# Kernel optimization log

Hardware: AMD Instinct MI355X
Metric: run time of the kernel (lower is better)

## Reference

```python
import jax, jax.numpy as jnp
import numpy as np

N = 13627        # n_nodes (from negative_sampling call in source)
E_EDGES = 504378 # n_edges
F_IN = 64
H1, H2, LIN_H = 300, 100, 100  # CONFIG HIDDEN_1/HIDDEN_2/LINEAR_HIDDEN


def setup_inputs() -> dict:
    key = jax.random.key(0)
    ks = jax.random.split(key, 10)
    x = jax.random.normal(ks[0], (N, F_IN), jnp.float32)
    edge_index = jax.random.randint(ks[1], (2, E_EDGES), 0, N, dtype=jnp.int64)
    neg_edge_index = jax.random.randint(ks[2], (2, E_EDGES), 0, N, dtype=jnp.int64)
    def w(k, shape):
        return jax.random.normal(k, shape, jnp.float32) * 0.05
    return dict(
        x=x, edge_index=edge_index, neg_edge_index=neg_edge_index,
        W1=w(ks[3], (2, F_IN, H1)), b1=jnp.zeros((H1,), jnp.float32),
        W2=w(ks[4], (2, H1, H2)), b2=jnp.zeros((H2,), jnp.float32),
        W3=w(ks[5], (2, H2, 1)), b3=jnp.zeros((1,), jnp.float32),
        linW1=w(ks[6], (F_IN, LIN_H)), linb1=jnp.zeros((LIN_H,), jnp.float32),
        linW2=w(ks[7], (F_IN, LIN_H)), linb2=jnp.zeros((LIN_H,), jnp.float32),
        c1=jnp.array([0.5], jnp.float32), c2=jnp.array([0.5], jnp.float32),
    )


def _cheb_norm(edge_index, n):
    # PyG ChebConv sym normalization with lambda_max=2: Lhat = L - I,
    # off-diagonal entries -deg[src]^-1/2 * deg[dst]^-1/2, diagonal 0.
    src, dst = edge_index[0], edge_index[1]
    deg = jax.ops.segment_sum(jnp.ones(src.shape, jnp.float32), src, num_segments=n)
    dinv = jnp.where(deg > 0, jax.lax.rsqrt(jnp.maximum(deg, 1.0)), 0.0)
    return -dinv[src] * dinv[dst]


def _cheb_conv(x, W, b, src, dst, norm, n):
    # K=2: out = Tx0 @ W[0] + Tx1 @ W[1] + b, with Tx1 = Lhat @ x (gather-scale-scatter)
    tx1 = jax.ops.segment_sum(norm[:, None] * x[src], dst, num_segments=n)
    return x @ W[0] + tx1 @ W[1] + b


def reference(x, edge_index, neg_edge_index, W1, b1, W2, b2, W3, b3,
              linW1, linb1, linW2, linb2, c1, c2):
    n = x.shape[0]
    src, dst = edge_index[0], edge_index[1]
    norm = _cheb_norm(edge_index, n)
    h = jax.nn.relu(_cheb_conv(x, W1, b1, src, dst, norm, n))
    x1 = jax.nn.relu(_cheb_conv(h, W2, b2, src, dst, norm, n))
    xo = x1 + jax.nn.relu(x @ linW1 + linb1)
    z = x1 + jax.nn.relu(x @ linW2 + linb2)
    pos = jax.nn.sigmoid(jnp.sum(z[edge_index[0]] * z[edge_index[1]], axis=1))
    pos_loss = -jnp.mean(jnp.log(pos + 1e-15))
    neg = jax.nn.sigmoid(jnp.sum(z[neg_edge_index[0]] * z[neg_edge_index[1]], axis=1))
    neg_loss = -jnp.mean(jnp.log(1.0 - neg + 1e-15))
    r_loss = pos_loss + neg_loss
    out = _cheb_conv(xo, W3, b3, src, dst, norm, n)
    return out, r_loss, c1, c2
```

## Files before the change

### kernel.cpp

```cpp
#include <hip/hip_runtime.h>
#include <math.h>


typedef unsigned short ushort_t;
typedef float v2f __attribute__((ext_vector_type(2)));
typedef short bf16x8 __attribute__((ext_vector_type(8)));
typedef float f32x4 __attribute__((ext_vector_type(4)));

#define GBM 64
#define GBN 64
#define GBK 32
#define LDK 72
#define HB  256
#define PACKN 6816

__device__ inline short f2bf(float f) {
    unsigned u = __float_as_uint(f);
    u += 0x7fff + ((u >> 16) & 1);
    return (short)(u >> 16);
}
__device__ inline float bflo(unsigned w) { return __uint_as_float(w << 16); }
__device__ inline float bfhi(unsigned w) { return __uint_as_float(w & 0xffff0000u); }

__device__ inline float dot16fp8(uint4 ra, uint4 rb) {
    float dot = 0.0f;
    v2f fa, fb;
    fa = __builtin_amdgcn_cvt_pk_f32_fp8(ra.x, false);
    fb = __builtin_amdgcn_cvt_pk_f32_fp8(rb.x, false);
    dot += fa.x * fb.x + fa.y * fb.y;
    fa = __builtin_amdgcn_cvt_pk_f32_fp8(ra.x, true);
    fb = __builtin_amdgcn_cvt_pk_f32_fp8(rb.x, true);
    dot += fa.x * fb.x + fa.y * fb.y;
    fa = __builtin_amdgcn_cvt_pk_f32_fp8(ra.y, false);
    fb = __builtin_amdgcn_cvt_pk_f32_fp8(rb.y, false);
    dot += fa.x * fb.x + fa.y * fb.y;
    fa = __builtin_amdgcn_cvt_pk_f32_fp8(ra.y, true);
    fb = __builtin_amdgcn_cvt_pk_f32_fp8(rb.y, true);
    dot += fa.x * fb.x + fa.y * fb.y;
    fa = __builtin_amdgcn_cvt_pk_f32_fp8(ra.z, false);
    fb = __builtin_amdgcn_cvt_pk_f32_fp8(rb.z, false);
    dot += fa.x * fb.x + fa.y * fb.y;
    fa = __builtin_amdgcn_cvt_pk_f32_fp8(ra.z, true);
    fb = __builtin_amdgcn_cvt_pk_f32_fp8(rb.z, true);
    dot += fa.x * fb.x + fa.y * fb.y;
    fa = __builtin_amdgcn_cvt_pk_f32_fp8(ra.w, false);
    fb = __builtin_amdgcn_cvt_pk_f32_fp8(rb.w, false);
    dot += fa.x * fb.x + fa.y * fb.y;
    fa = __builtin_amdgcn_cvt_pk_f32_fp8(ra.w, true);
    fb = __builtin_amdgcn_cvt_pk_f32_fp8(rb.w, true);
    dot += fa.x * fb.x + fa.y * fb.y;
    return dot;
}

__device__ inline float loss_term(float d, int y) {
    float sg = __builtin_amdgcn_rcpf(1.0f + __expf(-d));
    return y ? __logf(1.0f - sg + 1e-15f) : __logf(sg + 1e-15f);
}

__global__ __launch_bounds__(512) void hist_both_x_kernel(
    const int* __restrict__ ei, const float* __restrict__ x,
    int* __restrict__ degp, int* __restrict__ cntp,
    ushort_t* __restrict__ xb, int Nn, int E) {
    __shared__ int lhs[PACKN];
    __shared__ int lhd[PACKN];
    for (int i = threadIdx.x; i < PACKN; i += 512) { lhs[i] = 0; lhd[i] = 0; }
    __syncthreads();
    const int b = blockIdx.x;
    const int chunk = (E + HB - 1) / HB;
    const int e0 = b * chunk;
    const int e1 = (e0 + chunk < E) ? (e0 + chunk) : E;
    for (int e = e0 + threadIdx.x; e < e1; e += 512) {
        int s = ei[e], d = ei[E + e];
        atomicAdd(&lhs[s >> 1], 1 << ((s & 1) << 4));
        atomicAdd(&lhd[d >> 1], 1 << ((d & 1) << 4));
    }
    __syncthreads();
    int* ds = degp + (size_t)b * PACKN;
    int* cs = cntp + (size_t)b * PACKN;
    for (int i = threadIdx.x; i < PACKN; i += 512) { ds[i] = lhs[i]; cs[i] = lhd[i]; }
    const int rpb = (Nn + HB - 1) / HB;
    const int r0 = b * rpb;
    const int r1 = (r0 + rpb < Nn) ? (r0 + rpb) : Nn;
    for (int i = r0 * 64 + (int)threadIdx.x; i < r1 * 64; i += 512)
        xb[i] = (ushort_t)f2bf(x[i]);
}

__global__ void merge_kernel(const int* __restrict__ degp, const int* __restrict__ cntp,
                             ushort_t* __restrict__ off, int Nal,
                             float* __restrict__ dinv, int* __restrict__ rowptr,
                             float* __restrict__ acc, int n) {
    int tid = blockIdx.x * blockDim.x + threadIdx.x;
    if (tid == 0) {
        rowptr[0] = 0;
        acc[0] = 0.0f; acc[1] = 0.0f; acc[2] = 0.0f; acc[3] = 0.0f;
    }
    int v = tid >> 2, qq = tid & 3;
    if (v >= n) return;
    const int vh = v >> 1, sh = (v & 1) << 4;
    const int b0 = qq * (HB / 4), b1 = b0 + HB / 4;
    int dsum = 0, csum = 0;
    for (int b = b0; b < b1; ++b) {
        dsum += (degp[(size_t)b * PACKN + vh] >> sh) & 0xffff;
        csum += (cntp[(size_t)b * PACKN + vh] >> sh) & 0xffff;
    }
    int dtot = dsum;
    dtot += __shfl_xor(dtot, 1, 64);
    dtot += __shfl_xor(dtot, 2, 64);
    int inc = csum;
    int t = __shfl_up(inc, 1, 64); if (qq >= 1) inc += t;
    t = __shfl_up(inc, 2, 64);     if (qq >= 2) inc += t;
    int ex = inc - csum;
    if (qq == 0) dinv[v] = (dtot > 0) ? (1.0f / sqrtf((float)dtot)) : 0.0f;
    if (qq == 3) rowptr[v + 1] = inc;
    int run = ex;
    for (int b = b0; b < b1; ++b) {
        off[(size_t)b * Nal + v] = (ushort_t)run;
        run += (cntp[(size_t)b * PACKN + vh] >> sh) & 0xffff;
    }
}

__global__ void scan_kernel(int* __restrict__ rowptr, int n) {
    __shared__ int wsum[16];
    __shared__ int carry_s;
    if (threadIdx.x == 0) carry_s = 0;
    __syncthreads();
    int nchunk = (n + 1023) / 1024;
    int wid = threadIdx.x >> 6, lane = threadIdx.x & 63;
    for (int c = 0; c < nchunk; ++c) {
        int i = c * 1024 + threadIdx.x;
        int v = (i < n) ? rowptr[i + 1] : 0;
        int s = v;
        for (int off = 1; off < 64; off <<= 1) {
            int t = __shfl_up(s, off, 64);
            if (lane >= off) s += t;
        }
        if (lane == 63) wsum[wid] = s;
        __syncthreads();
        if (wid == 0 && lane < 16) {
            int wsv = wsum[lane];
            for (int off = 1; off < 16; off <<= 1) {
                int t = __shfl_up(wsv, off, 64);
                if (lane >= off) wsv += t;
            }
            wsum[lane] = wsv;
        }
        __syncthreads();
        int base = carry_s + (wid > 0 ? wsum[wid - 1] : 0);
        int inc = base + s;
        if (i < n) rowptr[i + 1] = inc;
        __syncthreads();
        if (threadIdx.x == 1023) carry_s = inc;
        __syncthreads();
    }
}

__global__ __launch_bounds__(512) void fill_lds_kernel(
    const int* __restrict__ ei, const float* __restrict__ dinv,
    const int* __restrict__ rowptr, const ushort_t* __restrict__ off, int Nal,
    int* __restrict__ colidx, float* __restrict__ wnorm, int E) {
    __shared__ int lh[PACKN];
    for (int i = threadIdx.x; i < PACKN; i += 512) lh[i] = 0;
    __syncthreads();
    const int b = blockIdx.x;
    const int chunk = (E + HB - 1) / HB;
    const int e0 = b * chunk;
    const int e1 = (e0 + chunk < E) ? (e0 + chunk) : E;
    const ushort_t* boff = off + (size_t)b * Nal;
    for (int e = e0 + threadIdx.x; e < e1; e += 512) {
        int s = ei[e], d = ei[E + e];
        int sh = (d & 1) << 4;
        int old = atomicAdd(&lh[d >> 1], 1 << sh);
        int rank = (old >> sh) & 0xffff;
        int slot = rowptr[d] + (int)boff[d] + rank;
        colidx[slot] = s;
        wnorm[slot] = -dinv[s] * dinv[d];
    }
}

__global__ void xt_kernel(const ushort_t* __restrict__ xb, const int* __restrict__ rowptr,
                          const int* __restrict__ colidx, const float* __restrict__ wnorm,
                          ushort_t* __restrict__ XTb, int n) {
    int node = (blockIdx.x * blockDim.x + threadIdx.x) >> 6;
    if (node >= n) return;
    int lane = threadIdx.x & 63;
    int grp = lane >> 4;
    int l = lane & 15;
    int j0 = rowptr[node], j1 = rowptr[node + 1];
    float a0 = 0, a1 = 0, a2 = 0, a3 = 0;
    int j = j0 + grp;
    if (j < j1) {
        float w = wnorm[j];
        int c = colidx[j];
        uint2 r = ((const uint2*)(xb + (size_t)c * 64))[l];
        for (;;) {
            int jn = j + 4;
            bool more = jn < j1;
            float wn = 0.0f;
            uint2 rn = r;
            if (more) {
                int cn = colidx[jn];
                wn = wnorm[jn];
                rn = ((const uint2*)(xb + (size_t)cn * 64))[l];
            }
            a0 += w * bflo(r.x); a1 += w * bfhi(r.x);
            a2 += w * bflo(r.y); a3 += w * bfhi(r.y);
            if (!more) break;
            j = jn; w = wn; r = rn;
        }
    }
    a0 += __shfl_xor(a0, 16, 64); a0 += __shfl_xor(a0, 32, 64);
    a1 += __shfl_xor(a1, 16, 64); a1 += __shfl_xor(a1, 32, 64);
    a2 += __shfl_xor(a2, 16, 64); a2 += __shfl_xor(a2, 32, 64);
    a3 += __shfl_xor(a3, 16, 64); a3 += __shfl_xor(a3, 32, 64);
    if (grp == 0) {
        uint2 xv = ((const uint2*)(xb + (size_t)node * 64))[l];
        *(uint2*)&XTb[(size_t)node * 128 + l * 4] = xv;
        uint2 p;
        p.x = (unsigned)(unsigned short)f2bf(a0) | ((unsigned)(unsigned short)f2bf(a1) << 16);
        p.y = (unsigned)(unsigned short)f2bf(a2) | ((unsigned)(unsigned short)f2bf(a3) << 16);
        *(uint2*)&XTb[(size_t)node * 128 + 64 + l * 4] = p;
    }
}

__global__ __launch_bounds__(256) void gemm_mfma(
    const ushort_t* __restrict__ Abf, int lda,
    const float* __restrict__ B0, const float* __restrict__ B1, const float* __restrict__ B2,
    const float* __restrict__ bias0, const float* __restrict__ bias1, const float* __restrict__ bias2,
    int split, int split2, int klim1,
    float* __restrict__ C, int ldc, ushort_t* __restrict__ Cbf, int ldcbf,
    int cbf_mode, int Nrows, int K, int Ncols, int relu) {
    __shared__ short As[GBM * LDK];
    __shared__ short Bs[GBN * LDK];
    const int bm = blockIdx.y * GBM, bn = blockIdx.x * GBN;
    const int tid = threadIdx.x;
    const int w = tid >> 6, l = tid & 63;
    const int wm = (w >> 1) * 32, wn = (w & 1) * 32;
    const int lr = l & 15;
    const int kg = l >> 4;
    const int arow = tid >> 2, aseg = tid & 3;
    const int bcol = tid & 63, bk2 = (tid >> 6) * 2;

    const int arowg = bm + arow;
    const int bcolg = bn + bcol;
    const float* Bsrc = nullptr;
    int ldb = 1, Klim = K;
    if (bcolg < split)                            { Bsrc = B0 + bcolg; ldb = split; Klim = K; }
    else if (bcolg < split2 && bcolg < Ncols)     { Bsrc = B1 + (bcolg - split); ldb = split2 - split; Klim = klim1; }
    else if (bcolg < Ncols)                       { Bsrc = B2 + (bcolg - split2); ldb = Ncols - split2; Klim = klim1; }

    f32x4 acc00 = {0,0,0,0}, acc01 = {0,0,0,0}, acc10 = {0,0,0,0}, acc11 = {0,0,0,0};

    for (int k0 = 0; k0 < K; k0 += GBK) {
        {
            int kk = k0 + aseg * 8;
            bf16x8 v;
            if (arowg < Nrows && kk + 7 < K) {
                v = *(const bf16x8*)&Abf[(size_t)arowg * lda + kk];
            } else {
#pragma unroll
                for (int i = 0; i < 8; ++i)
                    v[i] = (arowg < Nrows && kk + i < K)
                         ? (short)Abf[(size_t)arowg * lda + kk + i] : (short)0;
            }
            *(bf16x8*)&As[arow * LDK + aseg * 8] = v;
        }
#pragma unroll
        for (int q = 0; q < 4; ++q) {
            int k = q * 8 + bk2;
            unsigned pw = 0u;
            if (Bsrc) {
                float f0 = (k0 + k < Klim) ? Bsrc[(size_t)(k0 + k) * ldb] : 0.0f;
                float f1 = (k0 + k + 1 < Klim) ? Bsrc[(size_t)(k0 + k + 1) * ldb] : 0.0f;
                pw = (unsigned)(unsigned short)f2bf(f0)
                   | ((unsigned)(unsigned short)f2bf(f1) << 16);
            }
            *(unsigned*)&Bs[bcol * LDK + k] = pw;
        }
        __syncthreads();
        bf16x8 a0 = *(const bf16x8*)&As[(wm + lr) * LDK + kg * 8];
        bf16x8 a1 = *(const bf16x8*)&As[(wm + 16 + lr) * LDK + kg * 8];
        bf16x8 b0 = *(const bf16x8*)&Bs[(wn + lr) * LDK + kg * 8];
        bf16x8 b1 = *(const bf16x8*)&Bs[(wn + 16 + lr) * LDK + kg * 8];
        acc00 = __builtin_amdgcn_mfma_f32_16x16x32_bf16(a0, b0, acc00, 0, 0, 0);
        acc01 = __builtin_amdgcn_mfma_f32_16x16x32_bf16(a0, b1, acc01, 0, 0, 0);
        acc10 = __builtin_amdgcn_mfma_f32_16x16x32_bf16(a1, b0, acc10, 0, 0, 0);
        acc11 = __builtin_amdgcn_mfma_f32_16x16x32_bf16(a1, b1, acc11, 0, 0, 0);
        __syncthreads();
    }
#pragma unroll
    for (int i = 0; i < 2; ++i) {
        int rbase = bm + wm + i * 16 + kg * 4;
#pragma unroll
        for (int j = 0; j < 2; ++j) {
            int col = bn + wn + j * 16 + lr;
            if (col >= Ncols) continue;
            float bv;
            if (col < split)       bv = bias0 ? bias0[col] : 0.0f;
            else if (col < split2) bv = bias1 ? bias1[col - split] : 0.0f;
            else                   bv = bias2 ? bias2[col - split2] : 0.0f;
            f32x4 a = (i == 0) ? (j == 0 ? acc00 : acc01) : (j == 0 ? acc10 : acc11);
#pragma unroll
            for (int r = 0; r < 4; ++r) {
                int row = rbase + r;
                if (row >= Nrows) continue;
                float o = a[r] + bv;
                if (cbf_mode == 3) {
                    if (col < split)
                        Cbf[(size_t)row * ldcbf + col] = (ushort_t)f2bf(fmaxf(o, 0.0f));
                    else
                        C[(size_t)row * ldc + (col - split)] = o;
                } else if (cbf_mode == 2) {
                    if (relu) o = fmaxf(o, 0.0f);
                    Cbf[(size_t)row * ldcbf + col] = (ushort_t)f2bf(o);
                } else if (cbf_mode == 1 && col >= split) {
                    Cbf[(size_t)row * 128 + (col - split)] = (ushort_t)f2bf(o);
                } else {
                    if (relu) o = fmaxf(o, 0.0f);
                    C[(size_t)row * ldc + col] = o;
                }
            }
        }
    }
}

__global__ void segsum_combine1_kernel(const ushort_t* __restrict__ hb,
                                       const int* __restrict__ rowptr, const int* __restrict__ colidx,
                                       const float* __restrict__ wnorm,
                                       const float* __restrict__ G2a, const float* __restrict__ b2,
                                       float* __restrict__ x1, int n) {
    int node = (blockIdx.x * blockDim.x + threadIdx.x) >> 6;
    if (node >= n) return;
    int lane = threadIdx.x & 63;
    int grp = lane >> 4;
    int l = lane & 15;
    int j0 = rowptr[node], j1 = rowptr[node + 1];
    float acc[8] = {};
    int j = j0 + grp;
    if (j < j1) {
        float w = wnorm[j];
        int c = colidx[j];
        uint4 r = ((const uint4*)(hb + (size_t)c * 128))[l];
        for (;;) {
            int jn = j + 4;
            bool more = jn < j1;
            float wn = 0.0f;
            uint4 rn = r;
            if (more) {
                int cn = colidx[jn];
                wn = wnorm[jn];
                rn = ((const uint4*)(hb + (size_t)cn * 128))[l];
            }
            acc[0] += w * bflo(r.x); acc[1] += w * bfhi(r.x);
            acc[2] += w * bflo(r.y); acc[3] += w * bfhi(r.y);
            acc[4] += w * bflo(r.z); acc[5] += w * bfhi(r.z);
            acc[6] += w * bflo(r.w); acc[7] += w * bfhi(r.w);
            if (!more) break;
            j = jn; w = wn; r = rn;
        }
    }
#pragma unroll
    for (int k = 0; k < 8; ++k) {
        acc[k] += __shfl_xor(acc[k], 16, 64);
        acc[k] += __shfl_xor(acc[k], 32, 64);
    }
    if (grp == 0) {
        int f = l * 8;
        if (f < 100) {
            float4 g0 = *(const float4*)&G2a[(size_t)node * 100 + f];
            float4 bv0 = *(const float4*)&b2[f];
            float4 o0;
            o0.x = fmaxf(g0.x + acc[0] + bv0.x, 0.0f);
            o0.y = fmaxf(g0.y + acc[1] + bv0.y, 0.0f);
            o0.z = fmaxf(g0.z + acc[2] + bv0.z, 0.0f);
            o0.w = fmaxf(g0.w + acc[3] + bv0.w, 0.0f);
            *(float4*)&x1[(size_t)node * 100 + f] = o0;
            if (f + 8 <= 100) {
                float4 g1 = *(const float4*)&G2a[(size_t)node * 100 + f + 4];
                float4 bv1 = *(const float4*)&b2[f + 4];
                float4 o1;
                o1.x = fmaxf(g1.x + acc[4] + bv1.x, 0.0f);
                o1.y = fmaxf(g1.y + acc[5] + bv1.y, 0.0f);
                o1.z = fmaxf(g1.z + acc[6] + bv1.z, 0.0f);
                o1.w = fmaxf(g1.w + acc[7] + bv1.w, 0.0f);
                *(float4*)&x1[(size_t)node * 100 + f + 4] = o1;
            }
        }
    }
}

__global__ void combine2_kernel(const float* __restrict__ S, const float* __restrict__ x1,
                                const float* __restrict__ w3b,
                                float* __restrict__ xo, unsigned* __restrict__ zf,
                                float* __restrict__ sv, int n) {
    int idx = blockIdx.x * blockDim.x + threadIdx.x;
    if (idx >= n * 32) return;
    int i = idx >> 5, q = idx & 31;
    unsigned w = 0u;
    float part = 0.0f;
    if (q < 25) {
        float4 s1 = *(const float4*)&S[(size_t)i * 200 + q * 4];
        float4 s2 = *(const float4*)&S[(size_t)i * 200 + 100 + q * 4];
        float4 xv = *(const float4*)&x1[(size_t)i * 100 + q * 4];
        float4 a, b;
        a.x = xv.x + fmaxf(s1.x, 0.0f); a.y = xv.y + fmaxf(s1.y, 0.0f);
        a.z = xv.z + fmaxf(s1.z, 0.0f); a.w = xv.w + fmaxf(s1.w, 0.0f);
        b.x = xv.x + fmaxf(s2.x, 0.0f); b.y = xv.y + fmaxf(s2.y, 0.0f);
        b.z = xv.z + fmaxf(s2.z, 0.0f); b.w = xv.w + fmaxf(s2.w, 0.0f);
        *(float4*)&xo[(size_t)i * 100 + q * 4] = a;
        w = (unsigned)__builtin_amdgcn_cvt_pk_fp8_f32(b.x, b.y, 0, false);
        w = (unsigned)__builtin_amdgcn_cvt_pk_fp8_f32(b.z, b.w, (int)w, true);
        float4 wv = *(const float4*)&w3b[q * 4];
        part = a.x * wv.x + a.y * wv.y + a.z * wv.z + a.w * wv.w;
    }
    zf[(size_t)i * 32 + q] = w;
#pragma unroll
    for (int off = 16; off > 0; off >>= 1)
        part += __shfl_xor(part, off, 32);
    if (q == 0) sv[i] = part;
}

__global__ __launch_bounds__(256) void edge_loss_fp8_kernel(
    const unsigned* __restrict__ zf, const int* __restrict__ ei,
    const int* __restrict__ nei, int E, float* __restrict__ accv) {
    const int y = blockIdx.y;
    const int* __restrict__ lst = y ? nei : ei;
    const int l = threadIdx.x & 7;
    const int g = (blockIdx.x * blockDim.x + threadIdx.x) >> 3;
    const int ng = (gridDim.x * blockDim.x) >> 3;
    const int stride2 = 2 * ng;
    float s = 0.0f;
    const int gA = g, gB = g + ng;
    int niterA = (gA < E) ? ((E - 1 - gA) / stride2 + 1) : 0;
    int niterB = (gB < E) ? ((E - 1 - gB) / stride2 + 1) : 0;
    if (niterA > 0) {
        int eB0 = (gB < E) ? gB : (E - 1);
        int eA1 = (gA + stride2 < E) ? (gA + stride2) : (E - 1);
        int eB1 = (gB + stride2 < E) ? (gB + stride2) : (E - 1);
        int aA0 = lst[gA], bA0 = lst[E + gA];
        int aB0 = lst[eB0], bB0 = lst[E + eB0];
        int aA1 = lst[eA1], bA1 = lst[E + eA1];
        int aB1 = lst[eB1], bB1 = lst[E + eB1];
        uint4 raA = *(const uint4*)&zf[(size_t)aA0 * 32 + l * 4];
        uint4 rbA = *(const uint4*)&zf[(size_t)bA0 * 32 + l * 4];
        uint4 raB = *(const uint4*)&zf[(size_t)aB0 * 32 + l * 4];
        uint4 rbB = *(const uint4*)&zf[(size_t)bB0 * 32 + l * 4];
        for (int t = 0; t < niterA; ++t) {
            int eA2 = gA + (t + 2) * stride2; eA2 = (eA2 < E) ? eA2 : (E - 1);
            int eB2 = gB + (t + 2) * stride2; eB2 = (eB2 < E) ? eB2 : (E - 1);
            int aA2 = lst[eA2], bA2 = lst[E + eA2];
            int aB2 = lst[eB2], bB2 = lst[E + eB2];
            uint4 raA1 = *(const uint4*)&zf[(size_t)aA1 * 32 + l * 4];
            uint4 rbA1 = *(const uint4*)&zf[(size_t)bA1 * 32 + l * 4];
            uint4 raB1 = *(const uint4*)&zf[(size_t)aB1 * 32 + l * 4];
            uint4 rbB1 = *(const uint4*)&zf[(size_t)bB1 * 32 + l * 4];
            float dA = dot16fp8(raA, rbA);
            float dB = dot16fp8(raB, rbB);
            dA += __shfl_xor(dA, 1, 8); dB += __shfl_xor(dB, 1, 8);
            dA += __shfl_xor(dA, 2, 8); dB += __shfl_xor(dB, 2, 8);
            dA += __shfl_xor(dA, 4, 8); dB += __shfl_xor(dB, 4, 8);
            if (l == 0) {
                s += loss_term(dA, y);
                if (t < niterB) s += loss_term(dB, y);
            }
            aA1 = aA2; bA1 = bA2; aB1 = aB2; bB1 = bB2;
            raA = raA1; rbA = rbA1; raB = raB1; rbB = rbB1;
        }
    }
    __shared__ float red[256];
    red[threadIdx.x] = s;
    __syncthreads();
    for (int st = 128; st > 0; st >>= 1) {
        if (threadIdx.x < st) red[threadIdx.x] += red[threadIdx.x + st];
        __syncthreads();
    }
    if (threadIdx.x == 0) atomicAdd(&accv[y], red[0]);
}

__global__ void out_finalize_kernel(const float* __restrict__ xo, const float* __restrict__ W3,
                                    const float* __restrict__ b3, const int* __restrict__ rowptr,
                                    const int* __restrict__ colidx, const float* __restrict__ wnorm,
                                    const float* __restrict__ sv, const float* __restrict__ accv,
                                    const float* __restrict__ c1, const float* __restrict__ c2,
                                    float* __restrict__ out, int n, int E) {
    int i = blockIdx.x * blockDim.x + threadIdx.x;
    if (i == 0) {
        out[n]     = -(accv[0] + accv[1]) / (float)E;
        out[n + 1] = c1[0];
        out[n + 2] = c2[0];
    }
    if (i >= n) return;
    const float4* a = (const float4*)(xo + (size_t)i * 100);
    const float4* wv = (const float4*)W3;
    float acc = b3[0];
#pragma unroll
    for (int q = 0; q < 25; ++q) {
        float4 va = a[q], vw = wv[q];
        acc += va.x * vw.x + va.y * vw.y + va.z * vw.z + va.w * vw.w;
    }
    int j1 = rowptr[i + 1];
    for (int j = rowptr[i]; j < j1; ++j)
        acc += wnorm[j] * sv[colidx[j]];
    out[i] = acc;
}

extern "C" void kernel_launch(void* const* d_in, const int* in_sizes, int n_in,
                              void* d_out, int out_size, void* d_ws, size_t ws_size,
                              hipStream_t stream) {
    (void)n_in; (void)out_size; (void)ws_size;
    const float* x   = (const float*)d_in[0];
    const int*   ei  = (const int*)d_in[1];
    const int*   nei = (const int*)d_in[2];
    const float* W1  = (const float*)d_in[3];
    const float* b1  = (const float*)d_in[4];
    const float* W2  = (const float*)d_in[5];
    const float* b2  = (const float*)d_in[6];
    const float* W3  = (const float*)d_in[7];
    const float* b3  = (const float*)d_in[8];
    const float* lw1 = (const float*)d_in[9];
    const float* lb1 = (const float*)d_in[10];
    const float* lw2 = (const float*)d_in[11];
    const float* lb2 = (const float*)d_in[12];
    const float* c1  = (const float*)d_in[13];
    const float* c2  = (const float*)d_in[14];

    const int Nn = in_sizes[0] / 64;
    const int E  = in_sizes[1] / 2;

    const size_t Nal = ((size_t)Nn + 5) & ~(size_t)3;
    const size_t Eal = ((size_t)E + 3) & ~(size_t)3;
    const int LDH = 304;

    float* ws       = (float*)d_ws;
    float* acc      = ws;
    float* dinv     = acc + 4;
    int*   rowptr   = (int*)(dinv + Nal);
    int*   colidx   = rowptr + Nal;
    float* wnorm    = (float*)(colidx + Eal);
    int*   degp     = (int*)(wnorm + Eal);
    int*   cntp     = degp + (size_t)HB * PACKN;
    ushort_t* offus = (ushort_t*)(cntp + (size_t)HB * PACKN);
    ushort_t* xb    = offus + (size_t)HB * Nal;
    ushort_t* XTb   = xb + (size_t)Nn * 64;
    ushort_t* hb    = XTb + (size_t)Nn * 128;
    float* G2a      = (float*)(hb + (size_t)Nn * LDH);
    float* x1       = G2a + (size_t)Nn * 100;
    float* xo       = x1 + (size_t)Nn * 100;
    float* S        = xo + (size_t)Nn * 100;
    size_t zoff     = (size_t)(S + (size_t)Nn * 200 - ws);
    zoff = (zoff + 31) & ~(size_t)31;
    unsigned* zf    = (unsigned*)(ws + zoff);
    size_t hoff2    = zoff + (size_t)Nn * 32 + 63;
    hoff2 &= ~(size_t)63;
    ushort_t* hWb   = (ushort_t*)(ws + hoff2);
    float* sv       = ws + hoff2 + (size_t)Nn * 64;
    const int MB = (Nn + GBM - 1) / GBM;

    hist_both_x_kernel<<<HB, 512, 0, stream>>>(ei, x, degp, cntp, xb, Nn, E);
    merge_kernel<<<(4 * Nn + 255) / 256, 256, 0, stream>>>(degp, cntp, offus, (int)Nal,
                                                           dinv, rowptr, acc, Nn);
    scan_kernel<<<1, 1024, 0, stream>>>(rowptr, Nn);
    fill_lds_kernel<<<HB, 512, 0, stream>>>(ei, dinv, rowptr, offus, (int)Nal,
                                            colidx, wnorm, E);

    xt_kernel<<<(Nn + 3) / 4, 256, 0, stream>>>(xb, rowptr, colidx, wnorm, XTb, Nn);
    gemm_mfma<<<dim3(8, MB), 256, 0, stream>>>(
        XTb, 128, W1, lw1, lw2, b1, lb1, lb2,
        300, 400, 64, S, 200, hb, LDH, 3, Nn, 128, 500, 1);

    gemm_mfma<<<dim3(4, MB), 256, 0, stream>>>(
        hb, LDH, W2, W2 + 300 * 100, W2 + 300 * 100, nullptr, nullptr, nullptr,
        100, 200, 300, G2a, 100, hWb, 0, 1, Nn, 300, 200, 0);
    segsum_combine1_kernel<<<(Nn + 3) / 4, 256, 0, stream>>>(hWb, rowptr, colidx, wnorm,
                                                             G2a, b2, x1, Nn);

    combine2_kernel<<<(Nn * 32 + 255) / 256, 256, 0, stream>>>(S, x1, W3 + 100,
                                                               xo, zf, sv, Nn);

    edge_loss_fp8_kernel<<<dim3(1024, 2), 256, 0, stream>>>(zf, ei, nei, E, acc);

    out_finalize_kernel<<<(Nn + 255) / 256, 256, 0, stream>>>(
        xo, W3, b3, rowptr, colidx, wnorm, sv, acc, c1, c2, (float*)d_out, Nn, E);
}
```

Baseline: 206.8 us.

## Pre-pack weights to transposed bf16 and drop LDS staging in GEMMs

Adds a kernel that converts W1, the two linear weights and W2 once into padded, transposed bf16 matrices, with a fused bias vector. The GEMM is rewritten so each wave loads its MFMA operands straight from global memory, with no shared-memory staging and no barriers. This removes the strided fp32 weight loads and the per-tile bf16 conversion that every block used to repeat. In exchange it adds an extra launch, pads the hidden buffer to 320 columns, and relies on caches to absorb the operand loads that waves now fetch redundantly.

```diff
diff --git a/kernel.cpp b/kernel.cpp
--- a/kernel.cpp
+++ b/kernel.cpp
@@ -7,12 +7,9 @@
 typedef short bf16x8 __attribute__((ext_vector_type(8)));
 typedef float f32x4 __attribute__((ext_vector_type(4)));
 
-#define GBM 64
-#define GBN 64
-#define GBK 32
-#define LDK 72
 #define HB  256
 #define PACKN 6816
+#define LDH 320
 
 __device__ inline short f2bf(float f) {
     unsigned u = __float_as_uint(f);
@@ -55,6 +52,38 @@
 __device__ inline float loss_term(float d, int y) {
     float sg = __builtin_amdgcn_rcpf(1.0f + __expf(-d));
     return y ? __logf(1.0f - sg + 1e-15f) : __logf(sg + 1e-15f);
+}
+
+__global__ void pack_weights_kernel(const float* __restrict__ W1, const float* __restrict__ b1,
+                                    const float* __restrict__ lw1, const float* __restrict__ lb1,
+                                    const float* __restrict__ lw2, const float* __restrict__ lb2,
+                                    const float* __restrict__ W2,
+                                    ushort_t* __restrict__ BtA, float* __restrict__ ba,
+                                    ushort_t* __restrict__ BtB) {
+    int tid = blockIdx.x * blockDim.x + threadIdx.x;
+    int stride = gridDim.x * blockDim.x;
+    for (int i = tid; i < 576 * 128; i += stride) {
+        int r = i >> 7, k = i & 127;
+        float v = 0.0f;
+        if (r < 300) v = W1[(size_t)k * 300 + r];
+        else if (r >= 320 && r < 420) { if (k < 64) v = lw1[k * 100 + (r - 320)]; }
+        else if (r >= 420 && r < 520) { if (k < 64) v = lw2[k * 100 + (r - 420)]; }
+        BtA[i] = (ushort_t)f2bf(v);
+    }
+    for (int i = tid; i < 576; i += stride) {
+        float v = 0.0f;
+        if (i < 300) v = b1[i];
+        else if (i >= 320 && i < 420) v = lb1[i - 320];
+        else if (i >= 420 && i < 520) v = lb2[i - 420];
+        ba[i] = v;
+    }
+    for (int i = tid; i < 256 * 320; i += stride) {
+        int r = i / 320, k = i - r * 320;
+        float v = 0.0f;
+        if (k < 300 && r < 200)
+            v = (r < 100) ? W2[(size_t)k * 100 + r] : W2[30000 + (size_t)k * 100 + (r - 100)];
+        BtB[i] = (ushort_t)f2bf(v);
+    }
 }
 
 __global__ __launch_bounds__(512) void hist_both_x_kernel(
@@ -222,70 +251,32 @@
     }
 }
 
-__global__ __launch_bounds__(256) void gemm_mfma(
+__global__ __launch_bounds__(256) void gemm_direct(
     const ushort_t* __restrict__ Abf, int lda,
-    const float* __restrict__ B0, const float* __restrict__ B1, const float* __restrict__ B2,
-    const float* __restrict__ bias0, const float* __restrict__ bias1, const float* __restrict__ bias2,
-    int split, int split2, int klim1,
+    const ushort_t* __restrict__ Bt, int ldbt,
+    const float* __restrict__ bias,
     float* __restrict__ C, int ldc, ushort_t* __restrict__ Cbf, int ldcbf,
-    int cbf_mode, int Nrows, int K, int Ncols, int relu) {
-    __shared__ short As[GBM * LDK];
-    __shared__ short Bs[GBN * LDK];
-    const int bm = blockIdx.y * GBM, bn = blockIdx.x * GBN;
+    int mode, int split, int Nrows, int Kp, int Ncols) {
+    const int bm = blockIdx.y * 64, bn = blockIdx.x * 64;
     const int tid = threadIdx.x;
     const int w = tid >> 6, l = tid & 63;
     const int wm = (w >> 1) * 32, wn = (w & 1) * 32;
-    const int lr = l & 15;
-    const int kg = l >> 4;
-    const int arow = tid >> 2, aseg = tid & 3;
-    const int bcol = tid & 63, bk2 = (tid >> 6) * 2;
-
-    const int arowg = bm + arow;
-    const int bcolg = bn + bcol;
-    const float* Bsrc = nullptr;
-    int ldb = 1, Klim = K;
-    if (bcolg < split)                            { Bsrc = B0 + bcolg; ldb = split; Klim = K; }
-    else if (bcolg < split2 && bcolg < Ncols)     { Bsrc = B1 + (bcolg - split); ldb = split2 - split; Klim = klim1; }
-    else if (bcolg < Ncols)                       { Bsrc = B2 + (bcolg - split2); ldb = Ncols - split2; Klim = klim1; }
-
+    const int lr = l & 15, kg = l >> 4;
+    const ushort_t* pa0 = Abf + (size_t)(bm + wm + lr) * lda + kg * 8;
+    const ushort_t* pa1 = pa0 + (size_t)16 * lda;
+    const ushort_t* pb0 = Bt + (size_t)(bn + wn + lr) * ldbt + kg * 8;
+    const ushort_t* pb1 = pb0 + (size_t)16 * ldbt;
     f32x4 acc00 = {0,0,0,0}, acc01 = {0,0,0,0}, acc10 = {0,0,0,0}, acc11 = {0,0,0,0};
-
-    for (int k0 = 0; k0 < K; k0 += GBK) {
-        {
-            int kk = k0 + aseg * 8;
-            bf16x8 v;
-            if (arowg < Nrows && kk + 7 < K) {
-                v = *(const bf16x8*)&Abf[(size_t)arowg * lda + kk];
-            } else {
-#pragma unroll
-                for (int i = 0; i < 8; ++i)
-                    v[i] = (arowg < Nrows && kk + i < K)
-                         ? (short)Abf[(size_t)arowg * lda + kk + i] : (short)0;
-            }
-            *(bf16x8*)&As[arow * LDK + aseg * 8] = v;
-        }
-#pragma unroll
-        for (int q = 0; q < 4; ++q) {
-            int k = q * 8 + bk2;
-            unsigned pw = 0u;
-            if (Bsrc) {
-                float f0 = (k0 + k < Klim) ? Bsrc[(size_t)(k0 + k) * ldb] : 0.0f;
-                float f1 = (k0 + k + 1 < Klim) ? Bsrc[(size_t)(k0 + k + 1) * ldb] : 0.0f;
-                pw = (unsigned)(unsigned short)f2bf(f0)
-                   | ((unsigned)(unsigned short)f2bf(f1) << 16);
-            }
-            *(unsigned*)&Bs[bcol * LDK + k] = pw;
-        }
-        __syncthreads();
-        bf16x8 a0 = *(const bf16x8*)&As[(wm + lr) * LDK + kg * 8];
-        bf16x8 a1 = *(const bf16x8*)&As[(wm + 16 + lr) * LDK + kg * 8];
-        bf16x8 b0 = *(const bf16x8*)&Bs[(wn + lr) * LDK + kg * 8];
-        bf16x8 b1 = *(const bf16x8*)&Bs[(wn + 16 + lr) * LDK + kg * 8];
+#pragma unroll 2
+    for (int k0 = 0; k0 < Kp; k0 += 32) {
+        bf16x8 a0 = *(const bf16x8*)(pa0 + k0);
+        bf16x8 a1 = *(const bf16x8*)(pa1 + k0);
+        bf16x8 b0 = *(const bf16x8*)(pb0 + k0);
+        bf16x8 b1 = *(const bf16x8*)(pb1 + k0);
         acc00 = __builtin_amdgcn_mfma_f32_16x16x32_bf16(a0, b0, acc00, 0, 0, 0);
         acc01 = __builtin_amdgcn_mfma_f32_16x16x32_bf16(a0, b1, acc01, 0, 0, 0);
         acc10 = __builtin_amdgcn_mfma_f32_16x16x32_bf16(a1, b0, acc10, 0, 0, 0);
         acc11 = __builtin_amdgcn_mfma_f32_16x16x32_bf16(a1, b1, acc11, 0, 0, 0);
-        __syncthreads();
     }
 #pragma unroll
     for (int i = 0; i < 2; ++i) {
@@ -294,36 +285,30 @@
         for (int j = 0; j < 2; ++j) {
             int col = bn + wn + j * 16 + lr;
             if (col >= Ncols) continue;
-            float bv;
-            if (col < split)       bv = bias0 ? bias0[col] : 0.0f;
-            else if (col < split2) bv = bias1 ? bias1[col - split] : 0.0f;
-            else                   bv = bias2 ? bias2[col - split2] : 0.0f;
+            float bv = bias ? bias[col] : 0.0f;
             f32x4 a = (i == 0) ? (j == 0 ? acc00 : acc01) : (j == 0 ? acc10 : acc11);
 #pragma unroll
             for (int r = 0; r < 4; ++r) {
                 int row = rbase + r;
                 if (row >= Nrows) continue;
                 float o = a[r] + bv;
-                if (cbf_mode == 3) {
+                if (mode == 3) {
                     if (col < split)
                         Cbf[(size_t)row * ldcbf + col] = (ushort_t)f2bf(fmaxf(o, 0.0f));
                     else
                         C[(size_t)row * ldc + (col - split)] = o;
-                } else if (cbf_mode == 2) {
-                    if (relu) o = fmaxf(o, 0.0f);
-                    Cbf[(size_t)row * ldcbf + col] = (ushort_t)f2bf(o);
-                } else if (cbf_mode == 1 && col >= split) {
-                    Cbf[(size_t)row * 128 + (col - split)] = (ushort_t)f2bf(o);
                 } else {
-                    if (relu) o = fmaxf(o, 0.0f);
-                    C[(size_t)row * ldc + col] = o;
+                    if (col < split)
+                        C[(size_t)row * ldc + col] = o;
+                    else
+                        Cbf[(size_t)row * 128 + (col - split)] = (ushort_t)f2bf(o);
                 }
             }
         }
     }
 }
 
-__global__ void segsum_combine1_kernel(const ushort_t* __restrict__ hb,
+__global__ void segsum_combine1_kernel(const ushort_t* __restrict__ hbw,
                                        const int* __restrict__ rowptr, const int* __restrict__ colidx,
                                        const float* __restrict__ wnorm,
                                        const float* __restrict__ G2a, const float* __restrict__ b2,
@@ -339,7 +324,7 @@
     if (j < j1) {
         float w = wnorm[j];
         int c = colidx[j];
-        uint4 r = ((const uint4*)(hb + (size_t)c * 128))[l];
+        uint4 r = ((const uint4*)(hbw + (size_t)c * 128))[l];
         for (;;) {
             int jn = j + 4;
             bool more = jn < j1;
@@ -348,7 +333,7 @@
             if (more) {
                 int cn = colidx[jn];
                 wn = wnorm[jn];
-                rn = ((const uint4*)(hb + (size_t)cn * 128))[l];
+                rn = ((const uint4*)(hbw + (size_t)cn * 128))[l];
             }
             acc[0] += w * bflo(r.x); acc[1] += w * bfhi(r.x);
             acc[2] += w * bflo(r.y); acc[3] += w * bfhi(r.y);
@@ -528,7 +513,8 @@
 
     const size_t Nal = ((size_t)Nn + 5) & ~(size_t)3;
     const size_t Eal = ((size_t)E + 3) & ~(size_t)3;
-    const int LDH = 304;
+    const int MB = (Nn + 63) / 64;
+    const size_t Nr = (size_t)MB * 64;
 
     float* ws       = (float*)d_ws;
     float* acc      = ws;
@@ -541,8 +527,11 @@
     ushort_t* offus = (ushort_t*)(cntp + (size_t)HB * PACKN);
     ushort_t* xb    = offus + (size_t)HB * Nal;
     ushort_t* XTb   = xb + (size_t)Nn * 64;
-    ushort_t* hb    = XTb + (size_t)Nn * 128;
-    float* G2a      = (float*)(hb + (size_t)Nn * LDH);
+    ushort_t* hbw   = XTb + Nr * 128;
+    ushort_t* BtA   = hbw + Nr * LDH;
+    ushort_t* BtB   = BtA + 576 * 128;
+    float* ba       = (float*)(BtB + 256 * 320);
+    float* G2a      = ba + 576;
     float* x1       = G2a + (size_t)Nn * 100;
     float* xo       = x1 + (size_t)Nn * 100;
     float* S        = xo + (size_t)Nn * 100;
@@ -553,7 +542,9 @@
     hoff2 &= ~(size_t)63;
     ushort_t* hWb   = (ushort_t*)(ws + hoff2);
     float* sv       = ws + hoff2 + (size_t)Nn * 64;
-    const int MB = (Nn + GBM - 1) / GBM;
+
+    pack_weights_kernel<<<256, 256, 0, stream>>>(W1, b1, lw1, lb1, lw2, lb2, W2,
+                                                 BtA, ba, BtB);
 
     hist_both_x_kernel<<<HB, 512, 0, stream>>>(ei, x, degp, cntp, xb, Nn, E);
     merge_kernel<<<(4 * Nn + 255) / 256, 256, 0, stream>>>(degp, cntp, offus, (int)Nal,
@@ -563,13 +554,11 @@
                                             colidx, wnorm, E);
 
     xt_kernel<<<(Nn + 3) / 4, 256, 0, stream>>>(xb, rowptr, colidx, wnorm, XTb, Nn);
-    gemm_mfma<<<dim3(8, MB), 256, 0, stream>>>(
-        XTb, 128, W1, lw1, lw2, b1, lb1, lb2,
-        300, 400, 64, S, 200, hb, LDH, 3, Nn, 128, 500, 1);
-
-    gemm_mfma<<<dim3(4, MB), 256, 0, stream>>>(
-        hb, LDH, W2, W2 + 300 * 100, W2 + 300 * 100, nullptr, nullptr, nullptr,
-        100, 200, 300, G2a, 100, hWb, 0, 1, Nn, 300, 200, 0);
+    gemm_direct<<<dim3(9, MB), 256, 0, stream>>>(
+        XTb, 128, BtA, 128, ba, S, 200, hbw, LDH, 3, 320, Nn, 128, 520);
+
+    gemm_direct<<<dim3(4, MB), 256, 0, stream>>>(
+        hbw, LDH, BtB, 320, nullptr, G2a, 100, hWb, 0, 1, 100, Nn, 320, 200);
     segsum_combine1_kernel<<<(Nn + 3) / 4, 256, 0, stream>>>(hWb, rowptr, colidx, wnorm,
                                                              G2a, b2, x1, Nn);
 
```

After: 213.6 us. 3.3% more time.
